# Performance work log

Measured on AMD Instinct MI355X. Metric: run time of the kernel, lower is better.

The kernel has to match this reference:

```python
import jax, jax.numpy as jnp
import numpy as np

B, T, S = 256, 32, 128
I, H, O = 256, 1024, 256


def setup_inputs() -> dict:
    key = jax.random.key(0)
    ks = jax.random.split(key, 8)
    sc = 0.02
    return {
        "shifted_target": jax.random.normal(ks[0], (B, T, I), jnp.float32),
        "encoder_outputs": jax.random.normal(ks[1], (B, S, H), jnp.float32),
        "W_ih": jax.random.normal(ks[2], (4 * H, I), jnp.float32) * sc,
        "W_hh": jax.random.normal(ks[3], (4 * H, H), jnp.float32) * sc,
        "b_ih": jax.random.normal(ks[4], (4 * H,), jnp.float32) * sc,
        "b_hh": jax.random.normal(ks[5], (4 * H,), jnp.float32) * sc,
        "W_fc": jax.random.normal(ks[6], (O, 2 * H), jnp.float32) * sc,
        "b_fc": jax.random.normal(ks[7], (O,), jnp.float32) * sc,
    }


def reference(shifted_target, encoder_outputs, W_ih, W_hh, b_ih, b_hh, W_fc, b_fc):
    bs, tgt_len, inp = shifted_target.shape
    hid = encoder_outputs.shape[-1]
    # torch code feeds zeros (not shifted_target[:,0]) at t=0, with zero init state
    xs = shifted_target.at[:, 0, :].set(0.0)
    xs = jnp.swapaxes(xs, 0, 1)  # [T, B, I]

    def step(carry, x_t):
        h, c = carry
        gates = x_t @ W_ih.T + b_ih + h @ W_hh.T + b_hh  # [B, 4H]
        i, f, g, o = jnp.split(gates, 4, axis=-1)
        i = jax.nn.sigmoid(i)
        f = jax.nn.sigmoid(f)
        g = jnp.tanh(g)
        o = jax.nn.sigmoid(o)
        c = f * c + i * g
        h = o * jnp.tanh(c)
        # dot-product attention against encoder states
        score = jnp.einsum('bh,bsh->bs', h, encoder_outputs)
        prob = jax.nn.softmax(score, axis=-1)
        ctx = jnp.einsum('bs,bsh->bh', prob, encoder_outputs)
        out_t = jnp.concatenate([ctx, h], axis=-1) @ W_fc.T + b_fc
        return (h, c), (out_t, prob)

    h0 = jnp.zeros((bs, hid), shifted_target.dtype)
    c0 = jnp.zeros((bs, hid), shifted_target.dtype)
    _, (outs, probs) = jax.lax.scan(step, (h0, c0), xs)
    return jnp.swapaxes(outs, 0, 1), jnp.swapaxes(probs, 0, 1)
```

## Files before the change

kernel.cpp:

```cpp
#include <hip/hip_runtime.h>
#include <math.h>

#define B_  256
#define T_  32
#define S_  128
#define I_  256
#define H_  1024
#define O_  256
#define G4  4096
#define K2  2048

typedef __attribute__((ext_vector_type(8))) short bf16x8;
typedef __attribute__((ext_vector_type(4))) float f32x4;

#define MFMA16(a, b, c) __builtin_amdgcn_mfma_f32_16x16x32_bf16(a, b, c, 0, 0, 0)

__device__ __forceinline__ unsigned short f2bf(float f) {
    unsigned int u = __float_as_uint(f);
    u = (u + 0x7FFFu + ((u >> 16) & 1u)) >> 16;
    return (unsigned short)u;
}
__device__ __forceinline__ float sigm(float x) { return 1.0f / (1.0f + __expf(-x)); }

__device__ __forceinline__ bf16x8 ldg_sys(const unsigned short* p) {
    bf16x8 r;
    asm volatile("global_load_dwordx4 %0, %1, off sc0 sc1"
                 : "=v"(r) : "v"(p) : "memory");
    return r;
}
__device__ __forceinline__ void stg_sys16(unsigned short* p, unsigned short v) {
    asm volatile("global_store_short %0, %1, off sc0 sc1"
                 :: "v"(p), "v"(v) : "memory");
}
__device__ __forceinline__ unsigned ldg_flag(const unsigned* p) {
    unsigned r;
    asm volatile("global_load_dword %0, %1, off sc0 sc1\n\ts_waitcnt vmcnt(0)"
                 : "=v"(r) : "v"(p) : "memory");
    return r;
}
__device__ __forceinline__ void stg_flag(unsigned* p, unsigned v) {
    asm volatile("global_store_dword %0, %1, off sc0 sc1"
                 :: "v"(p), "v"(v) : "memory");
}

__global__ void prep_kernel(
    const float* __restrict__ x, const float* __restrict__ enc,
    const float* __restrict__ Wih, const float* __restrict__ Whh,
    const float* __restrict__ bih, const float* __restrict__ bhh,
    const float* __restrict__ Wfc,
    unsigned short* __restrict__ WihR, unsigned short* __restrict__ WhhR,
    unsigned short* __restrict__ WfcR, float* __restrict__ biasR,
    unsigned short* __restrict__ xs, unsigned short* __restrict__ encB,
    unsigned short* __restrict__ h0, unsigned short* __restrict__ h1,
    unsigned* __restrict__ bar)
{
    if (blockIdx.x == 0 && threadIdx.x < 256) bar[threadIdx.x] = 0u;

    const long NWHH = (long)G4 * H_;
    const long NWIH = (long)G4 * I_;
    const long NWFC = (long)O_ * K2;
    const long NB   = G4;
    const long NX   = (long)B_ * T_ * I_;
    const long NE   = (long)B_ * S_ * H_;
    const long NH   = (long)B_ * H_;
    const long total = NWHH + NWIH + NWFC + NB + NX + NE + 2 * NH;
    for (long i = (long)blockIdx.x * blockDim.x + threadIdx.x; i < total;
         i += (long)gridDim.x * blockDim.x) {
        long j = i;
        if (j < NE) { encB[j] = f2bf(enc[j]); continue; }
        j -= NE;
        if (j < NWHH) {
            int r = (int)(j >> 10), k = (int)(j & 1023);
            int n = ((r & 1023) << 2) | (r >> 10);
            WhhR[(long)n * H_ + k] = f2bf(Whh[j]);
            continue;
        }
        j -= NWHH;
        if (j < NWIH) {
            int r = (int)(j >> 8), k = (int)(j & 255);
            int n = ((r & 1023) << 2) | (r >> 10);
            WihR[(long)n * I_ + k] = f2bf(Wih[j]);
            continue;
        }
        j -= NWIH;
        if (j < NWFC) { WfcR[j] = f2bf(Wfc[j]); continue; }
        j -= NWFC;
        if (j < NB) {
            int r = (int)j;
            int n = ((r & 1023) << 2) | (r >> 10);
            biasR[n] = bih[r] + bhh[r];
            continue;
        }
        j -= NB;
        if (j < NX) {
            int t = (int)((j >> 8) & 31);
            xs[j] = (t == 0) ? (unsigned short)0 : f2bf(x[j]);
            continue;
        }
        j -= NX;
        if (j < NH) { h0[j] = 0; continue; }
        j -= NH;
        h1[j] = 0;
    }
}

__global__ __launch_bounds__(512, 2) void steps_kernel(
    const unsigned short* __restrict__ xs,
    const unsigned short* __restrict__ WihR,
    const unsigned short* __restrict__ WhhR,
    const float* __restrict__ biasR,
    unsigned short* __restrict__ h0b,
    unsigned short* __restrict__ h1b,
    unsigned short* __restrict__ hall,
    unsigned* __restrict__ bar)
{
    __shared__ unsigned short Wlds[64 * 1024];
    __shared__ float Gs[64 * 68];

    const int tid = threadIdx.x;
    const int lane = tid & 63, wave = tid >> 6;
    const int quad = lane >> 4, l16 = lane & 15;
    const int wm = wave >> 2, wn = wave & 3;

    const int id = blockIdx.x;
    const int xcd = id & 7, slot = id >> 3;
    const int nt = slot >> 2, mt = slot & 3;
    const int n0 = (xcd * 8 + nt) * 64;
    const int m0 = mt * 64;

    unsigned* myflag = bar + mt * 64 + xcd * 8 + nt;
    const unsigned* gflags = bar + mt * 64;

    for (int i = 0; i < 16; i++) {
        int q = i * 512 + tid;
        int row = q >> 7, kc = q & 127;
        int e = kc * 8;
        int de = row * 1024 + (e ^ ((row & 7) << 3));
        *(uint4*)(Wlds + de) = *(const uint4*)(WhhR + (long)(n0 + row) * H_ + e);
    }

    const int nw = n0 + wn * 16 + l16;
    bf16x8 bwx[8];
    {
        const unsigned short* px = WihR + (long)nw * I_ + quad * 8;
#pragma unroll
        for (int kk = 0; kk < 8; kk++) bwx[kk] = *(const bf16x8*)(px + kk * 32);
    }
    const float bj = biasR[nw];

    const unsigned short* bbase = Wlds + (wn * 16 + l16) * 1024;
    const int swz = (l16 & 7) << 3;

    const unsigned short* xrow[2];
    long hoff[2];
#pragma unroll
    for (int i = 0; i < 2; i++) {
        int ar = m0 + wm * 32 + i * 16 + l16;
        xrow[i] = xs + (long)ar * T_ * I_ + quad * 8;
        hoff[i] = (long)ar * H_ + quad * 8;
    }

    float c_reg[2] = {0.f, 0.f};

    __syncthreads();

#pragma unroll 1
    for (int t = 0; t < T_; t++) {
        const unsigned short* hp = (t & 1) ? h1b : h0b;
        unsigned short* hn = (t & 1) ? h0b : h1b;

        const f32x4 z = {0.f, 0.f, 0.f, 0.f};
        f32x4 acc[2] = {z, z};

        {
            bf16x8 a[8][2];
#pragma unroll
            for (int kk = 0; kk < 8; kk++)
#pragma unroll
                for (int i = 0; i < 2; i++)
                    a[kk][i] = *(const bf16x8*)(xrow[i] + (long)t * I_ + kk * 32);
#pragma unroll
            for (int kk = 0; kk < 8; kk++)
#pragma unroll
                for (int i = 0; i < 2; i++)
                    acc[i] = MFMA16(a[kk][i], bwx[kk], acc[i]);
        }

        if (t > 0) {
            if (tid < 64) {
                int spins = 0;
                while (ldg_flag(gflags + tid) < (unsigned)t &&
                       spins < (1 << 20)) {
                    __builtin_amdgcn_s_sleep(1);
                    ++spins;
                }
            }
            __syncthreads();
            __builtin_amdgcn_sched_barrier(0);
        }

#pragma unroll
        for (int kc = 0; kc < 4; kc++) {
            bf16x8 a[8][2];
#pragma unroll
            for (int kk = 0; kk < 8; kk++)
#pragma unroll
                for (int i = 0; i < 2; i++)
                    a[kk][i] = ldg_sys(hp + hoff[i] + (long)(kc * 8 + kk) * 32);
            bf16x8 bb[8];
#pragma unroll
            for (int kk = 0; kk < 8; kk++) {
                int e = ((kc * 8 + kk) * 32 + quad * 8) ^ swz;
                bb[kk] = *(const bf16x8*)(bbase + e);
            }
            asm volatile("s_waitcnt vmcnt(0)" ::: "memory");
            __builtin_amdgcn_sched_barrier(0);
#pragma unroll
            for (int kk = 0; kk < 8; kk++)
#pragma unroll
                for (int i = 0; i < 2; i++)
                    acc[i] = MFMA16(a[kk][i], bb[kk], acc[i]);
        }

#pragma unroll
        for (int i = 0; i < 2; i++)
#pragma unroll
            for (int r = 0; r < 4; r++)
                Gs[(wm * 32 + i * 16 + quad * 4 + r) * 68 + wn * 16 + l16] =
                    acc[i][r] + bj;
        __syncthreads();

#pragma unroll
        for (int j = 0; j < 2; j++) {
            int p = j * 512 + tid;
            int row = p >> 4, u = p & 15;
            float gi = Gs[row * 68 + u * 4 + 0];
            float gf = Gs[row * 68 + u * 4 + 1];
            float gg = Gs[row * 68 + u * 4 + 2];
            float go = Gs[row * 68 + u * 4 + 3];
            int b = m0 + row;
            int jg = (n0 >> 2) + u;
            float ii = sigm(gi), ff = sigm(gf), g3 = tanhf(gg), oo = sigm(go);
            float cn = ff * c_reg[j] + ii * g3;
            float hh = oo * tanhf(cn);
            c_reg[j] = cn;
            unsigned short hb = f2bf(hh);
            stg_sys16(hn + (long)b * H_ + jg, hb);
            hall[((long)b * T_ + t) * H_ + jg] = hb;
        }

        if (t < T_ - 1) {
            asm volatile("s_waitcnt vmcnt(0)" ::: "memory");
            __syncthreads();
            if (tid == 0) stg_flag(myflag, (unsigned)(t + 1));
        }
    }
}

__global__ __launch_bounds__(256) void scores_kernel(
    const unsigned short* __restrict__ hall,
    const unsigned short* __restrict__ encB,
    float* __restrict__ probs,
    unsigned short* __restrict__ PB)
{
    __shared__ float Sc[32 * 132];

    const int tid = threadIdx.x;
    const int lane = tid & 63, wave = tid >> 6;
    const int quad = lane >> 4, l16 = lane & 15;
    const int b = blockIdx.x;
    const int nw = wave;

    const unsigned short* pa0 = hall + ((long)b * T_ + l16) * H_ + quad * 8;
    const unsigned short* pa1 = hall + ((long)b * T_ + 16 + l16) * H_ + quad * 8;
    const unsigned short* pb0 = encB + ((long)b * S_ + nw * 32 + l16) * H_ + quad * 8;
    const unsigned short* pb1 = pb0 + 16 * H_;

    const f32x4 z = {0.f, 0.f, 0.f, 0.f};
    f32x4 acc00 = z, acc01 = z, acc10 = z, acc11 = z;

#pragma unroll 4
    for (int k0 = 0; k0 < H_; k0 += 32) {
        bf16x8 a0 = *(const bf16x8*)(pa0 + k0);
        bf16x8 a1 = *(const bf16x8*)(pa1 + k0);
        bf16x8 b0 = *(const bf16x8*)(pb0 + k0);
        bf16x8 b1 = *(const bf16x8*)(pb1 + k0);
        acc00 = MFMA16(a0, b0, acc00);
        acc01 = MFMA16(a0, b1, acc01);
        acc10 = MFMA16(a1, b0, acc10);
        acc11 = MFMA16(a1, b1, acc11);
    }
#pragma unroll
    for (int r = 0; r < 4; r++) {
        int row0 = quad * 4 + r;
        int col0 = nw * 32 + l16;
        Sc[row0 * 132 + col0]            = acc00[r];
        Sc[row0 * 132 + col0 + 16]       = acc01[r];
        Sc[(row0 + 16) * 132 + col0]      = acc10[r];
        Sc[(row0 + 16) * 132 + col0 + 16] = acc11[r];
    }
    __syncthreads();
    for (int r = 0; r < 8; r++) {
        int row = wave * 8 + r;
        float v0 = Sc[row * 132 + lane];
        float v1 = Sc[row * 132 + 64 + lane];
        float mx = fmaxf(v0, v1);
#pragma unroll
        for (int off = 32; off > 0; off >>= 1) mx = fmaxf(mx, __shfl_xor(mx, off));
        float e0 = __expf(v0 - mx), e1 = __expf(v1 - mx);
        float s = e0 + e1;
#pragma unroll
        for (int off = 32; off > 0; off >>= 1) s += __shfl_xor(s, off);
        float inv = 1.0f / s;
        float p0 = e0 * inv, p1 = e1 * inv;
        long o = ((long)b * T_ + row) * S_;
        probs[o + lane] = p0;
        probs[o + 64 + lane] = p1;
        PB[o + lane] = f2bf(p0);
        PB[o + 64 + lane] = f2bf(p1);
    }
}

__global__ __launch_bounds__(256) void ctx_kernel(
    const unsigned short* __restrict__ encB,
    const unsigned short* __restrict__ PB,
    unsigned short* __restrict__ ctxo)
{
    __shared__ unsigned short Es[S_ * 256];

    const int tid = threadIdx.x;
    const int lane = tid & 63, wave = tid >> 6;
    const int quad = lane >> 4, l16 = lane & 15;
    const int b = blockIdx.x;
    const int h0 = blockIdx.y * 256;

    for (int i = tid; i < S_ * 32; i += 256) {
        int s = i >> 5, hc = (i & 31) * 8;
        *(uint4*)(Es + s * 256 + hc) =
            *(const uint4*)(encB + ((long)b * S_ + s) * H_ + h0 + hc);
    }
    bf16x8 a[2][4];
#pragma unroll
    for (int i = 0; i < 2; i++)
#pragma unroll
        for (int ks = 0; ks < 4; ks++)
            a[i][ks] = *(const bf16x8*)(PB + ((long)b * T_ + i * 16 + l16) * S_ +
                                        ks * 32 + quad * 8);
    __syncthreads();

    f32x4 acc[2][4];
    const f32x4 z = {0.f, 0.f, 0.f, 0.f};
#pragma unroll
    for (int i = 0; i < 2; i++)
#pragma unroll
        for (int j = 0; j < 4; j++) acc[i][j] = z;

    const int cw = wave * 64;
#pragma unroll
    for (int ks = 0; ks < 4; ks++) {
        const int kb = ks * 32 + quad * 8;
#pragma unroll
        for (int j = 0; j < 4; j++) {
            const int col = cw + j * 16 + l16;
            bf16x8 bb;
#pragma unroll
            for (int e = 0; e < 8; e++) bb[e] = (short)Es[(kb + e) * 256 + col];
            acc[0][j] = MFMA16(a[0][ks], bb, acc[0][j]);
            acc[1][j] = MFMA16(a[1][ks], bb, acc[1][j]);
        }
    }
#pragma unroll
    for (int i = 0; i < 2; i++)
#pragma unroll
        for (int j = 0; j < 4; j++)
#pragma unroll
            for (int r = 0; r < 4; r++) {
                int row = i * 16 + quad * 4 + r;
                int col = h0 + cw + j * 16 + l16;
                ctxo[((long)b * T_ + row) * H_ + col] = f2bf(acc[i][j][r]);
            }
}

__global__ __launch_bounds__(256) void fc_kernel(
    const unsigned short* __restrict__ ctxo,
    const unsigned short* __restrict__ hall,
    const unsigned short* __restrict__ WfcR,
    const float* __restrict__ bfc,
    float* __restrict__ out)
{
    __shared__ __align__(16) unsigned short As[64 * 40];
    __shared__ __align__(16) unsigned short Bs[128 * 40];

    const int tid = threadIdx.x;
    const int lane = tid & 63, wave = tid >> 6;
    const int wm = wave >> 1, wn = wave & 1;
    const int quad = lane >> 4, l16 = lane & 15;
    const int n0 = blockIdx.x * 128, m0 = blockIdx.y * 64;

    const int arow = tid >> 2, akc = (tid & 3) * 8;
    const int brow = tid >> 1, bkc = (tid & 1) * 16;

    f32x4 acc[2][4];
    const f32x4 z = {0.f, 0.f, 0.f, 0.f};
#pragma unroll
    for (int i = 0; i < 2; i++)
#pragma unroll
        for (int j = 0; j < 4; j++) acc[i][j] = z;

    for (int k0 = 0; k0 < K2; k0 += 32) {
        const unsigned short* asrc = (k0 < H_)
            ? ctxo + (long)(m0 + arow) * H_ + k0 + akc
            : hall + (long)(m0 + arow) * H_ + (k0 - H_) + akc;
        *(uint4*)(As + arow * 40 + akc) = *(const uint4*)asrc;
        const unsigned short* src = WfcR + (long)(n0 + brow) * K2 + k0 + bkc;
        *(uint4*)(Bs + brow * 40 + bkc)     = *(const uint4*)src;
        *(uint4*)(Bs + brow * 40 + bkc + 8) = *(const uint4*)(src + 8);
        __syncthreads();
        bf16x8 a0 = *(const bf16x8*)(As + (wm * 32 + l16) * 40 + quad * 8);
        bf16x8 a1 = *(const bf16x8*)(As + (wm * 32 + 16 + l16) * 40 + quad * 8);
#pragma unroll
        for (int j = 0; j < 4; j++) {
            bf16x8 bb = *(const bf16x8*)(Bs + (wn * 64 + j * 16 + l16) * 40 + quad * 8);
            acc[0][j] = MFMA16(a0, bb, acc[0][j]);
            acc[1][j] = MFMA16(a1, bb, acc[1][j]);
        }
        __syncthreads();
    }
#pragma unroll
    for (int i = 0; i < 2; i++)
#pragma unroll
        for (int j = 0; j < 4; j++)
#pragma unroll
            for (int r = 0; r < 4; r++) {
                int row = m0 + wm * 32 + i * 16 + quad * 4 + r;
                int col = n0 + wn * 64 + j * 16 + l16;
                out[(long)row * O_ + col] = acc[i][j][r] + bfc[col];
            }
}

extern "C" void kernel_launch(void* const* d_in, const int* in_sizes, int n_in,
                              void* d_out, int out_size, void* d_ws, size_t ws_size,
                              hipStream_t stream) {
    const float* x   = (const float*)d_in[0];
    const float* enc = (const float*)d_in[1];
    const float* Wih = (const float*)d_in[2];
    const float* Whh = (const float*)d_in[3];
    const float* bih = (const float*)d_in[4];
    const float* bhh = (const float*)d_in[5];
    const float* Wfc = (const float*)d_in[6];
    const float* bfc = (const float*)d_in[7];
    float* out = (float*)d_out;

    char* ws = (char*)d_ws;
    unsigned short* WIHR = (unsigned short*)(ws + 0);
    unsigned short* WHHR = (unsigned short*)(ws + 2097152);
    unsigned short* WFCR = (unsigned short*)(ws + 10485760);
    float*          BIAS = (float*)         (ws + 11534336);
    unsigned short* XS   = (unsigned short*)(ws + 11550720);
    unsigned short* H0   = (unsigned short*)(ws + 15745024);
    unsigned short* H1   = (unsigned short*)(ws + 16269312);
    unsigned*       BAR  = (unsigned*)      (ws + 16793600);
    unsigned short* HALL = (unsigned short*)(ws + 17842176);
    unsigned short* ENCB = (unsigned short*)(ws + 34619392);
    unsigned short* PB   = (unsigned short*)(ws + 101728256);
    unsigned short* CTX  = (unsigned short*)(ws + 103825408);

    prep_kernel<<<8192, 256, 0, stream>>>(x, enc, Wih, Whh, bih, bhh, Wfc,
                                          WIHR, WHHR, WFCR, BIAS, XS, ENCB,
                                          H0, H1, BAR);

    {
        void* args[] = {(void*)&XS, (void*)&WIHR, (void*)&WHHR, (void*)&BIAS,
                        (void*)&H0, (void*)&H1, (void*)&HALL, (void*)&BAR};
        hipLaunchCooperativeKernel(reinterpret_cast<void*>(steps_kernel),
                                   dim3(256), dim3(512), args, 0, stream);
    }

    scores_kernel<<<B_, 256, 0, stream>>>(HALL, ENCB,
                                          out + (long)B_ * T_ * O_, PB);
    ctx_kernel<<<dim3(B_, 4), 256, 0, stream>>>(ENCB, PB, CTX);
    fc_kernel<<<dim3(2, 128), 256, 0, stream>>>(CTX, HALL, WFCR, bfc, out);
}
```

Before: 1.010 ms.

## Read recurrent state from hall, coalesce h stores, double-buffer h loads

```diff
diff --git a/kernel.cpp b/kernel.cpp
--- a/kernel.cpp
+++ b/kernel.cpp
@@ -12,6 +12,7 @@
 
 typedef __attribute__((ext_vector_type(8))) short bf16x8;
 typedef __attribute__((ext_vector_type(4))) float f32x4;
+typedef __attribute__((ext_vector_type(4))) unsigned u32x4;
 
 #define MFMA16(a, b, c) __builtin_amdgcn_mfma_f32_16x16x32_bf16(a, b, c, 0, 0, 0)
 
@@ -22,14 +23,8 @@
 }
 __device__ __forceinline__ float sigm(float x) { return 1.0f / (1.0f + __expf(-x)); }
 
-__device__ __forceinline__ bf16x8 ldg_sys(const unsigned short* p) {
-    bf16x8 r;
-    asm volatile("global_load_dwordx4 %0, %1, off sc0 sc1"
-                 : "=v"(r) : "v"(p) : "memory");
-    return r;
-}
-__device__ __forceinline__ void stg_sys16(unsigned short* p, unsigned short v) {
-    asm volatile("global_store_short %0, %1, off sc0 sc1"
+__device__ __forceinline__ void stg_sys128(unsigned short* p, u32x4 v) {
+    asm volatile("global_store_dwordx4 %0, %1, off sc0 sc1"
                  :: "v"(p), "v"(v) : "memory");
 }
 __device__ __forceinline__ unsigned ldg_flag(const unsigned* p) {
@@ -51,7 +46,7 @@
     unsigned short* __restrict__ WihR, unsigned short* __restrict__ WhhR,
     unsigned short* __restrict__ WfcR, float* __restrict__ biasR,
     unsigned short* __restrict__ xs, unsigned short* __restrict__ encB,
-    unsigned short* __restrict__ h0, unsigned short* __restrict__ h1,
+    unsigned short* __restrict__ h0,
     unsigned* __restrict__ bar)
 {
     if (blockIdx.x == 0 && threadIdx.x < 256) bar[threadIdx.x] = 0u;
@@ -63,7 +58,7 @@
     const long NX   = (long)B_ * T_ * I_;
     const long NE   = (long)B_ * S_ * H_;
     const long NH   = (long)B_ * H_;
-    const long total = NWHH + NWIH + NWFC + NB + NX + NE + 2 * NH;
+    const long total = NWHH + NWIH + NWFC + NB + NX + NE + NH;
     for (long i = (long)blockIdx.x * blockDim.x + threadIdx.x; i < total;
          i += (long)gridDim.x * blockDim.x) {
         long j = i;
@@ -98,9 +93,7 @@
             continue;
         }
         j -= NX;
-        if (j < NH) { h0[j] = 0; continue; }
-        j -= NH;
-        h1[j] = 0;
+        h0[j] = 0;
     }
 }
 
@@ -109,13 +102,13 @@
     const unsigned short* __restrict__ WihR,
     const unsigned short* __restrict__ WhhR,
     const float* __restrict__ biasR,
-    unsigned short* __restrict__ h0b,
-    unsigned short* __restrict__ h1b,
+    const unsigned short* __restrict__ h0b,
     unsigned short* __restrict__ hall,
     unsigned* __restrict__ bar)
 {
     __shared__ unsigned short Wlds[64 * 1024];
     __shared__ float Gs[64 * 68];
+    __shared__ unsigned short Hs[64 * 16];
 
     const int tid = threadIdx.x;
     const int lane = tid & 63, wave = tid >> 6;
@@ -136,7 +129,7 @@
         int row = q >> 7, kc = q & 127;
         int e = kc * 8;
         int de = row * 1024 + (e ^ ((row & 7) << 3));
-        *(uint4*)(Wlds + de) = *(const uint4*)(WhhR + (long)(n0 + row) * H_ + e);
+        *(u32x4*)(Wlds + de) = *(const u32x4*)(WhhR + (long)(n0 + row) * H_ + e);
     }
 
     const int nw = n0 + wn * 16 + l16;
@@ -151,13 +144,12 @@
     const unsigned short* bbase = Wlds + (wn * 16 + l16) * 1024;
     const int swz = (l16 & 7) << 3;
 
+    int arow[2];
     const unsigned short* xrow[2];
-    long hoff[2];
 #pragma unroll
     for (int i = 0; i < 2; i++) {
-        int ar = m0 + wm * 32 + i * 16 + l16;
-        xrow[i] = xs + (long)ar * T_ * I_ + quad * 8;
-        hoff[i] = (long)ar * H_ + quad * 8;
+        arow[i] = m0 + wm * 32 + i * 16 + l16;
+        xrow[i] = xs + (long)arow[i] * T_ * I_ + quad * 8;
     }
 
     float c_reg[2] = {0.f, 0.f};
@@ -166,9 +158,6 @@
 
 #pragma unroll 1
     for (int t = 0; t < T_; t++) {
-        const unsigned short* hp = (t & 1) ? h1b : h0b;
-        unsigned short* hn = (t & 1) ? h0b : h1b;
-
         const f32x4 z = {0.f, 0.f, 0.f, 0.f};
         f32x4 acc[2] = {z, z};
 
@@ -196,30 +185,41 @@
                 }
             }
             __syncthreads();
-            __builtin_amdgcn_sched_barrier(0);
-        }
-
-#pragma unroll
-        for (int kc = 0; kc < 4; kc++) {
-            bf16x8 a[8][2];
-#pragma unroll
-            for (int kk = 0; kk < 8; kk++)
-#pragma unroll
-                for (int i = 0; i < 2; i++)
-                    a[kk][i] = ldg_sys(hp + hoff[i] + (long)(kc * 8 + kk) * 32);
-            bf16x8 bb[8];
-#pragma unroll
-            for (int kk = 0; kk < 8; kk++) {
-                int e = ((kc * 8 + kk) * 32 + quad * 8) ^ swz;
-                bb[kk] = *(const bf16x8*)(bbase + e);
+        }
+
+        const unsigned short* hb;
+        long hstr;
+        if (t == 0) { hb = h0b;                      hstr = H_; }
+        else        { hb = hall + (long)(t - 1) * H_; hstr = (long)T_ * H_; }
+        const unsigned short* rp0 = hb + (long)arow[0] * hstr + quad * 8;
+        const unsigned short* rp1 = hb + (long)arow[1] * hstr + quad * 8;
+
+        {
+            bf16x8 aa[2][4][2];
+#pragma unroll
+            for (int kk = 0; kk < 4; kk++) {
+                aa[0][kk][0] = *(const bf16x8*)(rp0 + kk * 32);
+                aa[0][kk][1] = *(const bf16x8*)(rp1 + kk * 32);
             }
-            asm volatile("s_waitcnt vmcnt(0)" ::: "memory");
-            __builtin_amdgcn_sched_barrier(0);
-#pragma unroll
-            for (int kk = 0; kk < 8; kk++)
-#pragma unroll
-                for (int i = 0; i < 2; i++)
-                    acc[i] = MFMA16(a[kk][i], bb[kk], acc[i]);
+#pragma unroll
+            for (int sc = 0; sc < 8; sc++) {
+                const int cur = sc & 1, nxt = cur ^ 1;
+                if (sc < 7) {
+                    const int kb = (sc + 1) * 4;
+#pragma unroll
+                    for (int kk = 0; kk < 4; kk++) {
+                        aa[nxt][kk][0] = *(const bf16x8*)(rp0 + (kb + kk) * 32);
+                        aa[nxt][kk][1] = *(const bf16x8*)(rp1 + (kb + kk) * 32);
+                    }
+                }
+#pragma unroll
+                for (int kk = 0; kk < 4; kk++) {
+                    int e = ((sc * 4 + kk) * 32 + quad * 8) ^ swz;
+                    bf16x8 bb = *(const bf16x8*)(bbase + e);
+                    acc[0] = MFMA16(aa[cur][kk][0], bb, acc[0]);
+                    acc[1] = MFMA16(aa[cur][kk][1], bb, acc[1]);
+                }
+            }
         }
 
 #pragma unroll
@@ -238,15 +238,20 @@
             float gf = Gs[row * 68 + u * 4 + 1];
             float gg = Gs[row * 68 + u * 4 + 2];
             float go = Gs[row * 68 + u * 4 + 3];
-            int b = m0 + row;
-            int jg = (n0 >> 2) + u;
             float ii = sigm(gi), ff = sigm(gf), g3 = tanhf(gg), oo = sigm(go);
             float cn = ff * c_reg[j] + ii * g3;
             float hh = oo * tanhf(cn);
             c_reg[j] = cn;
-            unsigned short hb = f2bf(hh);
-            stg_sys16(hn + (long)b * H_ + jg, hb);
-            hall[((long)b * T_ + t) * H_ + jg] = hb;
+            Hs[row * 16 + u] = f2bf(hh);
+        }
+        __syncthreads();
+
+        if (tid < 128) {
+            int row = tid >> 1, half = tid & 1;
+            u32x4 v = *(const u32x4*)(Hs + row * 16 + half * 8);
+            unsigned short* dst = hall +
+                ((long)(m0 + row) * T_ + t) * H_ + (n0 >> 2) + half * 8;
+            stg_sys128(dst, v);
         }
 
         if (t < T_ - 1) {
@@ -336,8 +341,8 @@
 
     for (int i = tid; i < S_ * 32; i += 256) {
         int s = i >> 5, hc = (i & 31) * 8;
-        *(uint4*)(Es + s * 256 + hc) =
-            *(const uint4*)(encB + ((long)b * S_ + s) * H_ + h0 + hc);
+        *(u32x4*)(Es + s * 256 + hc) =
+            *(const u32x4*)(encB + ((long)b * S_ + s) * H_ + h0 + hc);
     }
     bf16x8 a[2][4];
 #pragma unroll
@@ -411,10 +416,10 @@
         const unsigned short* asrc = (k0 < H_)
             ? ctxo + (long)(m0 + arow) * H_ + k0 + akc
             : hall + (long)(m0 + arow) * H_ + (k0 - H_) + akc;
-        *(uint4*)(As + arow * 40 + akc) = *(const uint4*)asrc;
+        *(u32x4*)(As + arow * 40 + akc) = *(const u32x4*)asrc;
         const unsigned short* src = WfcR + (long)(n0 + brow) * K2 + k0 + bkc;
-        *(uint4*)(Bs + brow * 40 + bkc)     = *(const uint4*)src;
-        *(uint4*)(Bs + brow * 40 + bkc + 8) = *(const uint4*)(src + 8);
+        *(u32x4*)(Bs + brow * 40 + bkc)     = *(const u32x4*)src;
+        *(u32x4*)(Bs + brow * 40 + bkc + 8) = *(const u32x4*)(src + 8);
         __syncthreads();
         bf16x8 a0 = *(const bf16x8*)(As + (wm * 32 + l16) * 40 + quad * 8);
         bf16x8 a1 = *(const bf16x8*)(As + (wm * 32 + 16 + l16) * 40 + quad * 8);
@@ -458,7 +463,6 @@
     float*          BIAS = (float*)         (ws + 11534336);
     unsigned short* XS   = (unsigned short*)(ws + 11550720);
     unsigned short* H0   = (unsigned short*)(ws + 15745024);
-    unsigned short* H1   = (unsigned short*)(ws + 16269312);
     unsigned*       BAR  = (unsigned*)      (ws + 16793600);
     unsigned short* HALL = (unsigned short*)(ws + 17842176);
     unsigned short* ENCB = (unsigned short*)(ws + 34619392);
@@ -467,13 +471,13 @@
 
     prep_kernel<<<8192, 256, 0, stream>>>(x, enc, Wih, Whh, bih, bhh, Wfc,
                                           WIHR, WHHR, WFCR, BIAS, XS, ENCB,
-                                          H0, H1, BAR);
+                                          H0, BAR);
 
     {
         void* args[] = {(void*)&XS, (void*)&WIHR, (void*)&WHHR, (void*)&BIAS,
-                        (void*)&H0, (void*)&H1, (void*)&HALL, (void*)&BAR};
-        hipLaunchCooperativeKernel(reinterpret_cast<void*>(steps_kernel),
-                                   dim3(256), dim3(512), args, 0, stream);
+                        (void*)&H0, (void*)&HALL, (void*)&BAR};
+        (void)hipLaunchCooperativeKernel(reinterpret_cast<void*>(steps_kernel),
+                                         dim3(256), dim3(512), args, 0, stream);
     }
 
     scores_kernel<<<B_, 256, 0, stream>>>(HALL, ENCB,
```

New measurement: 998.5 us. About the same (-1.1%).
